# Optimization experiments

Measured on AMD Instinct MI355X. Metric: run time of the kernel, lower is better.

## Reference

```python
import jax, jax.numpy as jnp
import numpy as np

BN_EPS = 1e-5

def _bn(x, gamma, beta, relu=True):
    # training-mode BatchNorm over all dims except channel (last)
    axes = tuple(range(x.ndim - 1))
    mu = jnp.mean(x, axes, keepdims=True)
    var = jnp.var(x, axes, keepdims=True)
    y = (x - mu) / jnp.sqrt(var + BN_EPS) * gamma + beta
    return jax.nn.relu(y) if relu else y

def _l2norm(x, eps):
    # F.normalize: x / max(||x||, eps)
    n = jnp.sqrt(jnp.sum(x * x, axis=-1, keepdims=True))
    return x / jnp.maximum(n, eps)

def setup_inputs() -> dict:
    key = jax.random.key(0)
    ks = jax.random.split(key, 16)
    B, N, H, W, C = 2, 512, 16, 32, 64
    IN_DIM = 10 + C + C + 2  # 140
    MLP3 = [128, 64]
    s = 0.02
    inp = {
        "warped_xyz": jax.random.normal(ks[0], (B, N, 3), jnp.float32),
        "warped_points": jax.random.normal(ks[1], (B, N, C), jnp.float32),
        "RF3": jax.random.normal(ks[2], (B, C, H, W), jnp.float32),
        "RF3_index": jax.random.normal(ks[3], (B, 3, H, W), jnp.float32),
        "lidar_z": jax.random.uniform(ks[4], (B, N, 1), jnp.float32),
        # conv1x1 stack (mlp3)
        "W1": jax.random.normal(ks[5], (IN_DIM, MLP3[0]), jnp.float32) * s,
        "b1": jnp.zeros((MLP3[0],), jnp.float32),
        "g1": jnp.ones((MLP3[0],), jnp.float32),
        "be1": jnp.zeros((MLP3[0],), jnp.float32),
        "W2": jax.random.normal(ks[6], (MLP3[0], MLP3[1]), jnp.float32) * s,
        "b2": jnp.zeros((MLP3[1],), jnp.float32),
        "g2": jnp.ones((MLP3[1],), jnp.float32),
        "be2": jnp.zeros((MLP3[1],), jnp.float32),
        # conv1d stack (mlp4 = [feats_dim//2], then 2 logits)
        "M1w": jax.random.normal(ks[7], (MLP3[1], MLP3[1] // 2), jnp.float32) * s,
        "M1b": jnp.zeros((MLP3[1] // 2,), jnp.float32),
        "M1g": jnp.ones((MLP3[1] // 2,), jnp.float32),
        "M1be": jnp.zeros((MLP3[1] // 2,), jnp.float32),
        "M2w": jax.random.normal(ks[8], (MLP3[1] // 2, 2), jnp.float32) * s,
        "M2b": jnp.zeros((2,), jnp.float32),
    }
    return inp

def reference(warped_xyz, warped_points, RF3, RF3_index, lidar_z,
              W1, b1, g1, be1, W2, b2, g2, be2,
              M1w, M1b, M1g, M1be, M2w, M2b):
    B, N, _ = warped_xyz.shape
    _, Ci, H, W_ = RF3.shape
    M = H * W_
    RF3_bnc = RF3.transpose(0, 2, 3, 1).reshape(B, M, Ci)          # [B,M,C]
    idx_bnc = RF3_index.transpose(0, 2, 3, 1).reshape(B, M, 3)     # [B,M,3]

    src_xyz = warped_xyz[:, :, None, :]                             # [B,N,1,3]
    dst_xyz = idx_bnc[:, None, :, :]                                # [B,1,M,3]
    euc = (src_xyz - dst_xyz)[..., :2]                              # [B,N,M,2]
    euc_norm = jnp.sqrt(euc[..., 0:1] ** 2 + euc[..., 1:2] ** 2)    # [B,N,M,1]

    xyz_z = (warped_xyz * lidar_z)[:, :, None, :]                   # [B,N,1,3]
    src_pts = warped_points[:, :, None, :]                          # [B,N,1,C]
    dst_pts = RF3_bnc[:, None, :, :]                                # [B,1,M,C]

    geom = jnp.concatenate([
        jnp.broadcast_to(xyz_z, (B, N, M, 3)),
        jnp.broadcast_to(src_pts[..., :2], (B, N, M, 2)),
        jnp.broadcast_to(dst_xyz[..., :2], (B, N, M, 2)),
        euc, euc_norm], axis=-1)                                    # [B,N,M,10]
    desc = jnp.concatenate([
        jnp.broadcast_to(src_pts, (B, N, M, Ci)),
        jnp.broadcast_to(dst_pts, (B, N, M, Ci))], axis=-1)         # [B,N,M,2C]

    # cal_sim: cosine sim between lidar feats (src) and image feats (dst)
    src_n = _l2norm(warped_points, 1e-12)
    dst_n = _l2norm(RF3_bnc, 1e-12)
    cos = jnp.einsum('bnc,bmc->bnm', src_n, dst_n)                  # [B,N,M]
    s1 = cos / (jnp.max(cos, axis=2, keepdims=True) + 1e-6)         # src->dst norm
    s2 = cos / (jnp.max(cos, axis=1, keepdims=True) + 1e-10)        # dst->src norm
    sim = jnp.stack([s1, s2], axis=-1)                              # [B,N,M,2]

    feats = jnp.concatenate([geom, desc, sim], axis=-1)             # [B,N,M,140]
    feats = _bn(jnp.einsum('bnmi,io->bnmo', feats, W1) + b1, g1, be1)
    feats = _bn(jnp.einsum('bnmi,io->bnmo', feats, W2) + b2, g2, be2)

    aw = jax.nn.softmax(jnp.max(feats, axis=-1), axis=-1)           # [B,N,M]
    att = jnp.einsum('bnm,bnmc->bnc', aw, feats)                    # [B,N,C]

    att = _bn(att @ M1w + M1b, M1g, M1be)
    logits = att @ M2w + M2b                                        # [B,N,2]
    return logits
```

## Files before the change

kernel.cpp:

```cpp
#include <hip/hip_runtime.h>
#include <hip/hip_bf16.h>

#define B_ 2
#define N_ 512
#define M_ 512
#define C_ 64
#define O1 128
#define O2 64
#define O3 32
#define PBIG 524288.0f
#define P3   1024.0f

typedef short s8v __attribute__((ext_vector_type(8)));
typedef float f4v __attribute__((ext_vector_type(4)));

#define WS_SRCN 0
#define WS_DSTN 65536
#define WS_P0   0
#define WS_U    131072
#define WS_Z    131072
#define WS_V    262144
#define WS_DXY  393216
#define WS_COS  395264
#define WS_RMAX 919552
#define WS_ST1  920576
#define WS_ST2  936960
#define WS_ST3  945152
#define WS_CMAX 949248
#define WS_W2F  950272
#define WS_W9S  954368
#define WS_X2   961536

__device__ __forceinline__ unsigned short f2bf(float f){
  unsigned u = __float_as_uint(f);
  unsigned r = (u + 0x7fffu + ((u >> 16) & 1u)) >> 16;
  return (unsigned short)r;
}
__device__ __forceinline__ float bf2f(unsigned short h){
  return __uint_as_float(((unsigned)h) << 16);
}
__device__ __forceinline__ unsigned pk2(float lo, float hi){
  return (unsigned)f2bf(lo) | ((unsigned)f2bf(hi) << 16);
}
__device__ __forceinline__ unsigned pk_trunc(float lo, float hi){
  return __builtin_amdgcn_perm(__float_as_uint(hi), __float_as_uint(lo), 0x07060302u);
}
__device__ __forceinline__ f4v relu4(f4v z){
  z[0] = fmaxf(z[0], 0.f); z[1] = fmaxf(z[1], 0.f);
  z[2] = fmaxf(z[2], 0.f); z[3] = fmaxf(z[3], 0.f);
  return z;
}

__global__ __launch_bounds__(128) void k1(const float* __restrict__ wxyz,
    const float* __restrict__ wpts, const float* __restrict__ lz,
    const float* __restrict__ rf3, const float* __restrict__ rf3i,
    const float* __restrict__ W1, float* __restrict__ ws){
  int t = threadIdx.x;
  if (blockIdx.x < 1024){
    int blk = blockIdx.x; int b = blk >> 9, n = blk & 511;
    int bn = b*N_ + n;
    __shared__ float wp[64]; __shared__ float sxyz[3]; __shared__ float slz; __shared__ float srn;
    if (t < 64) wp[t] = wpts[bn*64 + t];
    if (t >= 64 && t < 67) sxyz[t-64] = wxyz[bn*3 + (t-64)];
    if (t == 67) slz = lz[bn];
    __syncthreads();
    if (t < 64){
      float v = wp[t]*wp[t];
      v += __shfl_down(v,32); v += __shfl_down(v,16); v += __shfl_down(v,8);
      v += __shfl_down(v,4);  v += __shfl_down(v,2);  v += __shfl_down(v,1);
      if (t == 0) srn = 1.0f / fmaxf(sqrtf(v), 1e-12f);
    }
    __syncthreads();
    if (t < 64) ws[WS_SRCN + bn*64 + t] = wp[t]*srn;
    int o = t;
    float x = sxyz[0], y = sxyz[1], z = sxyz[2], l = slz;
    float acc = x*l*W1[0*O1+o] + y*l*W1[1*O1+o] + z*l*W1[2*O1+o]
              + wp[0]*W1[3*O1+o] + wp[1]*W1[4*O1+o]
              + x*W1[7*O1+o] + y*W1[8*O1+o];
    #pragma unroll 8
    for (int c = 0; c < 64; ++c) acc += wp[c]*W1[(10+c)*O1+o];
    ws[WS_U + bn*O1 + o] = acc;
  } else {
    int blk = blockIdx.x - 1024; int b = blk >> 9, m = blk & 511;
    int bm = b*M_ + m;
    __shared__ float rf[64]; __shared__ float sdx, sdy, srn2;
    if (t < 64) rf[t] = rf3[(b*64 + t)*512 + m];
    if (t == 64) sdx = rf3i[(b*3 + 0)*512 + m];
    if (t == 65) sdy = rf3i[(b*3 + 1)*512 + m];
    __syncthreads();
    if (t < 64){
      float v = rf[t]*rf[t];
      v += __shfl_down(v,32); v += __shfl_down(v,16); v += __shfl_down(v,8);
      v += __shfl_down(v,4);  v += __shfl_down(v,2);  v += __shfl_down(v,1);
      if (t == 0) srn2 = 1.0f / fmaxf(sqrtf(v), 1e-12f);
    }
    __syncthreads();
    if (t < 64) ws[WS_DSTN + bm*64 + t] = rf[t]*srn2;
    if (t == 0){ ws[WS_DXY + bm*2+0] = sdx; ws[WS_DXY + bm*2+1] = sdy; }
    int o = t;
    float acc = sdx*(W1[5*O1+o] - W1[7*O1+o]) + sdy*(W1[6*O1+o] - W1[8*O1+o]);
    #pragma unroll 8
    for (int c = 0; c < 64; ++c) acc += rf[c]*W1[(74+c)*O1+o];
    ws[WS_V + bm*O1 + o] = acc;
  }
}

__global__ __launch_bounds__(256) void k2(float* __restrict__ ws){
  int blk = blockIdx.x; int b = blk >> 9, n = blk & 511; int t = threadIdx.x;
  int bn = b*N_ + n;
  __shared__ __align__(16) float sn[64];
  __shared__ float dnt[64*65];
  __shared__ float part[4*64];
  if (t < 64) sn[t] = ws[WS_SRCN + bn*64 + t];
  float lmax = -3.4e38f;
  for (int chunk = 0; chunk < 8; ++chunk){
    __syncthreads();
    const float4* src = (const float4*)(ws + WS_DSTN + (size_t)(b*M_ + chunk*64)*64);
    #pragma unroll
    for (int i = 0; i < 4; ++i){
      float4 v = src[t + i*256];
      int base = (t + i*256)*4; int mm = base >> 6, c = base & 63;
      float* dp = &dnt[mm*65 + c];
      dp[0]=v.x; dp[1]=v.y; dp[2]=v.z; dp[3]=v.w;
    }
    __syncthreads();
    {
      int mm = t & 63, cg = t >> 6;
      const float* dr = &dnt[mm*65 + cg*16];
      const float* sr = &sn[cg*16];
      float p = 0.f;
      #pragma unroll
      for (int k = 0; k < 16; ++k) p += sr[k]*dr[k];
      part[cg*64 + mm] = p;
    }
    __syncthreads();
    if (t < 64){
      float d = part[t] + part[64+t] + part[128+t] + part[192+t];
      ws[WS_COS + bn*M_ + chunk*64 + t] = d;
      lmax = fmaxf(lmax, d);
    }
  }
  if (t < 64){
    lmax = fmaxf(lmax, __shfl_xor(lmax,32)); lmax = fmaxf(lmax, __shfl_xor(lmax,16));
    lmax = fmaxf(lmax, __shfl_xor(lmax,8));  lmax = fmaxf(lmax, __shfl_xor(lmax,4));
    lmax = fmaxf(lmax, __shfl_xor(lmax,2));  lmax = fmaxf(lmax, __shfl_xor(lmax,1));
    if (t == 0) ws[WS_RMAX + bn] = 1.0f / (lmax + 1e-6f);
  }
}

__global__ __launch_bounds__(256) void k2r(float* __restrict__ ws){
  int blk = blockIdx.x;
  int b = blk >> 4; int c0 = (blk & 15)*32;
  int t = threadIdx.x;
  int col = c0 + (t & 31), seg = t >> 5;
  float mx = -3.4e38f;
  #pragma unroll 8
  for (int i = 0; i < 64; ++i){
    int n = seg*64 + i;
    mx = fmaxf(mx, ws[WS_COS + (size_t)(b*N_ + n)*M_ + col]);
  }
  __shared__ float sred[256];
  sred[t] = mx;
  __syncthreads();
  if (t < 32){
    float m2 = sred[t];
    #pragma unroll
    for (int s2 = 1; s2 < 8; ++s2) m2 = fmaxf(m2, sred[s2*32 + t]);
    ws[WS_CMAX + b*M_ + c0 + t] = 1.0f / (m2 + 1e-10f);
  }
}

__global__ __launch_bounds__(256) void k3(const float* __restrict__ wxyz,
    const float* __restrict__ W1, const float* __restrict__ b1, float* __restrict__ ws){
  int blk = blockIdx.x; int bn = blk >> 1, half = blk & 1; int t = threadIdx.x;
  int b = bn >> 9; int mbase = half*256;
  __shared__ float s_en[256], s_s1[256], s_s2[256];
  __shared__ float sred[512];
  float sx = wxyz[bn*3+0], sy = wxyz[bn*3+1];
  float ri = ws[WS_RMAX + bn];
  {
    int m = mbase + t;
    float2 d = *(const float2*)(ws + WS_DXY + (size_t)(b*M_+m)*2);
    float ex = sx-d.x, ey = sy-d.y;
    s_en[t] = sqrtf(ex*ex + ey*ey);
    float cv = ws[WS_COS + (size_t)bn*M_ + m];
    s_s1[t] = cv*ri;
    s_s2[t] = cv*ws[WS_CMAX + b*M_ + m];
  }
  __syncthreads();
  int o = t & 127, mh = t >> 7;
  float u  = ws[WS_U + bn*O1 + o] + b1[o];
  float w9 = W1[9*O1+o], wa = W1[138*O1+o], wb = W1[139*O1+o];
  float sum = 0.f, ssq = 0.f;
  const float* Vp = ws + WS_V + (size_t)b*M_*O1 + o;
  int lBeg = mh*128, lEnd = lBeg + 128;
  #pragma unroll 8
  for (int ml = lBeg; ml < lEnd; ++ml){
    float xv = u + Vp[(size_t)(mbase+ml)*O1] + s_en[ml]*w9 + s_s1[ml]*wa + s_s2[ml]*wb;
    sum += xv; ssq += xv*xv;
  }
  sred[mh*128 + o] = sum;
  sred[256 + mh*128 + o] = ssq;
  __syncthreads();
  if (t < 128){
    float S = sred[t] + sred[128+t];
    float Q = sred[256+t] + sred[384+t];
    int rep = blk & 63;
    atomicAdd(&ws[WS_ST1 + rep*256 + t], S);
    atomicAdd(&ws[WS_ST1 + rep*256 + 128 + t], Q);
  }
}

__global__ __launch_bounds__(128) void k3b(const float* __restrict__ W1,
    const float* __restrict__ b1, const float* __restrict__ g1,
    const float* __restrict__ be1, const float* __restrict__ W2, float* __restrict__ ws){
  int blk = blockIdx.x; int t = threadIdx.x;
  int o = t;
  float s = 0.f, q = 0.f;
  #pragma unroll 8
  for (int r = 0; r < 64; ++r){ s += ws[WS_ST1 + r*256 + o]; q += ws[WS_ST1 + r*256 + 128 + o]; }
  float mu = s/PBIG, var = q/PBIG - mu*mu;
  float istd = rsqrtf(var + 1e-5f);
  float A1 = g1[o]*istd, C1 = be1[o] - mu*A1;
  if (blk < 1024){
    int bn = blk;
    ws[WS_P0 + bn*O1 + o] = (ws[WS_U + bn*O1 + o] + b1[o])*A1 + C1;
  } else if (blk < 1040){
    int r0 = (blk - 1024)*64;
    for (int r = 0; r < 64; ++r)
      ws[WS_V + (size_t)(r0 + r)*O1 + o] *= A1;
  } else {
    ws[WS_W9S + o]       = W1[9*O1+o]*A1;
    ws[WS_W9S + 128 + o] = W1[138*O1+o]*A1;
    ws[WS_W9S + 256 + o] = W1[139*O1+o]*A1;
    unsigned short* wf = (unsigned short*)(ws + WS_W2F);
    for (int i = t; i < 8192; i += 128){
      int j = i & 7, ll = (i >> 3) & 63, ct = (i >> 9) & 3, k0q = i >> 11;
      int oo = k0q*32 + (ll >> 4)*8 + j, c = ct*16 + (ll & 15);
      wf[i] = f2bf(W2[oo*O2 + c]);
    }
  }
}

__global__ __launch_bounds__(256, 4) void k4(const float* __restrict__ wxyz,
    float* __restrict__ ws){
  int blk = blockIdx.x; int bn = blk >> 1, half = blk & 1;
  int b = bn >> 9; int t = threadIdx.x;
  __shared__ __align__(16) unsigned short wBf[8192];
  __shared__ __align__(16) float p0s[128], w9s[128], was[128], wbs[128];
  __shared__ float ls[64], lq[64];
  {
    const s8v* g = (const s8v*)(ws + WS_W2F);
    s8v* l = (s8v*)wBf;
    #pragma unroll
    for (int c2 = 0; c2 < 4; ++c2) l[c2*256 + t] = g[c2*256 + t];
  }
  if (t < 64){ ls[t] = 0.f; lq[t] = 0.f; }
  if (t < 128){
    p0s[t] = ws[WS_P0 + bn*O1 + t];
    w9s[t] = ws[WS_W9S + t];
    was[t] = ws[WS_W9S + 128 + t];
    wbs[t] = ws[WS_W9S + 256 + t];
  }
  __syncthreads();
  int ll = t & 63, w = t >> 6, l16 = ll & 15, quad = ll >> 4;
  float sx = wxyz[bn*3+0], sy = wxyz[bn*3+1];
  float ri = ws[WS_RMAX + bn];
  float sst[4][4], sq2[4][4];
  #pragma unroll
  for (int i = 0; i < 4; ++i)
    #pragma unroll
    for (int j = 0; j < 4; ++j){ sst[i][j] = 0.f; sq2[i][j] = 0.f; }
  uint4* xf4 = (uint4*)(ws + WS_X2) + (size_t)bn*4096;
  union U8 { s8v v; unsigned u[4]; };
  #pragma unroll
  for (int mci = 0; mci < 2; ++mci){
    int mc = half*2 + mci;
    int mA = mc*128 + w*32 + l16, mB = mA + 16;
    float2 dA = *(const float2*)(ws + WS_DXY + (size_t)(b*M_+mA)*2);
    float2 dB = *(const float2*)(ws + WS_DXY + (size_t)(b*M_+mB)*2);
    float cvA = ws[WS_COS + (size_t)bn*M_ + mA], cvB = ws[WS_COS + (size_t)bn*M_ + mB];
    float ciA = ws[WS_CMAX + b*M_ + mA],         ciB = ws[WS_CMAX + b*M_ + mB];
    float exA = sx-dA.x, eyA = sy-dA.y; float en0 = sqrtf(exA*exA + eyA*eyA);
    float exB = sx-dB.x, eyB = sy-dB.y; float en1 = sqrtf(exB*exB + eyB*eyB);
    float s10 = cvA*ri, s20 = cvA*ciA;
    float s11 = cvB*ri, s21 = cvB*ciB;
    const float* vpA = ws + WS_V + (size_t)(b*M_+mA)*O1;
    const float* vpB = ws + WS_V + (size_t)(b*M_+mB)*O1;
    f4v acc[2][4];
    #pragma unroll
    for (int i = 0; i < 2; ++i)
      #pragma unroll
      for (int j = 0; j < 4; ++j) acc[i][j] = (f4v){0.f,0.f,0.f,0.f};
    #pragma unroll
    for (int k0q = 0; k0q < 4; ++k0q){
      int ko = k0q*32 + quad*8;
      f4v p0a = *(const f4v*)&p0s[ko], p0b = *(const f4v*)&p0s[ko+4];
      f4v w9a = *(const f4v*)&w9s[ko], w9b = *(const f4v*)&w9s[ko+4];
      f4v waa = *(const f4v*)&was[ko], wab = *(const f4v*)&was[ko+4];
      f4v wba = *(const f4v*)&wbs[ko], wbb = *(const f4v*)&wbs[ko+4];
      f4v vA0 = *(const f4v*)(vpA + ko), vA1 = *(const f4v*)(vpA + ko + 4);
      f4v vB0 = *(const f4v*)(vpB + ko), vB1 = *(const f4v*)(vpB + ko + 4);
      f4v zaA = relu4(p0a + vA0 + en0*w9a + s10*waa + s20*wba);
      f4v zbA = relu4(p0b + vA1 + en0*w9b + s10*wab + s20*wbb);
      f4v zaB = relu4(p0a + vB0 + en1*w9a + s11*waa + s21*wba);
      f4v zbB = relu4(p0b + vB1 + en1*w9b + s11*wab + s21*wbb);
      U8 uA, uB;
      uA.u[0] = pk_trunc(zaA[0], zaA[1]); uA.u[1] = pk_trunc(zaA[2], zaA[3]);
      uA.u[2] = pk_trunc(zbA[0], zbA[1]); uA.u[3] = pk_trunc(zbA[2], zbA[3]);
      uB.u[0] = pk_trunc(zaB[0], zaB[1]); uB.u[1] = pk_trunc(zaB[2], zaB[3]);
      uB.u[2] = pk_trunc(zbB[0], zbB[1]); uB.u[3] = pk_trunc(zbB[2], zbB[3]);
      #pragma unroll
      for (int ct = 0; ct < 4; ++ct){
        s8v bb = *(const s8v*)&wBf[((k0q*4 + ct)*64 + ll)*8];
        acc[0][ct] = __builtin_amdgcn_mfma_f32_16x16x32_bf16(bb, uA.v, acc[0][ct], 0,0,0);
        acc[1][ct] = __builtin_amdgcn_mfma_f32_16x16x32_bf16(bb, uB.v, acc[1][ct], 0,0,0);
      }
    }
    #pragma unroll
    for (int mt = 0; mt < 2; ++mt){
      uint4 u0, u1;
      u0.x = pk2(acc[mt][0][0], acc[mt][0][1]); u0.y = pk2(acc[mt][0][2], acc[mt][0][3]);
      u0.z = pk2(acc[mt][1][0], acc[mt][1][1]); u0.w = pk2(acc[mt][1][2], acc[mt][1][3]);
      u1.x = pk2(acc[mt][2][0], acc[mt][2][1]); u1.y = pk2(acc[mt][2][2], acc[mt][2][3]);
      u1.z = pk2(acc[mt][3][0], acc[mt][3][1]); u1.w = pk2(acc[mt][3][2], acc[mt][3][3]);
      xf4[((((mc*4 + w)*2 + mt)*2 + 0)*64) + ll] = u0;
      xf4[((((mc*4 + w)*2 + mt)*2 + 1)*64) + ll] = u1;
    }
    #pragma unroll
    for (int ct = 0; ct < 4; ++ct)
      #pragma unroll
      for (int r = 0; r < 4; ++r){
        float a0 = acc[0][ct][r], a1 = acc[1][ct][r];
        sst[ct][r] += a0 + a1;
        sq2[ct][r] += a0*a0 + a1*a1;
      }
  }
  #pragma unroll
  for (int ct = 0; ct < 4; ++ct){
    #pragma unroll
    for (int r = 0; r < 4; ++r){
      float s = sst[ct][r], q = sq2[ct][r];
      s += __shfl_xor(s,1); s += __shfl_xor(s,2); s += __shfl_xor(s,4); s += __shfl_xor(s,8);
      q += __shfl_xor(q,1); q += __shfl_xor(q,2); q += __shfl_xor(q,4); q += __shfl_xor(q,8);
      if (l16 == 0){
        atomicAdd(&ls[ct*16 + quad*4 + r], s);
        atomicAdd(&lq[ct*16 + quad*4 + r], q);
      }
    }
  }
  __syncthreads();
  int rep = blk & 63;
  if (t < 64) atomicAdd(&ws[WS_ST2 + rep*128 + t], ls[t]);
  else if (t < 128) atomicAdd(&ws[WS_ST2 + rep*128 + t], lq[t-64]);
}

__global__ __launch_bounds__(256) void k5(const float* __restrict__ g2,
    const float* __restrict__ be2, const float* __restrict__ M1w,
    const float* __restrict__ M1b, float* __restrict__ ws){
  int bn = blockIdx.x; int t = threadIdx.x;
  __shared__ float sa2[64], sc2[64];
  __shared__ float s_mx[512];
  __shared__ float s_aw[512];
  __shared__ float red[256];
  __shared__ float part[64*65];
  __shared__ float s_att[64];
  __shared__ float sgmax, sinvS;
  if (t < 64){
    float s = 0.f, q = 0.f;
    #pragma unroll 8
    for (int r = 0; r < 64; ++r){ s += ws[WS_ST2 + r*128 + t]; q += ws[WS_ST2 + r*128 + 64 + t]; }
    float mu = s/PBIG, var = q/PBIG - mu*mu;
    float istd = rsqrtf(var + 1e-5f);
    float A2 = g2[t]*istd;
    sa2[t] = A2; sc2[t] = be2[t] - mu*A2;
  }
  __syncthreads();
  int ll = t & 63, w = t >> 6, l16 = ll & 15, quad = ll >> 4;
  const uint4* xf4 = (const uint4*)(ws + WS_X2) + (size_t)bn*4096;
  uint4 xv[4][2][2];
  #pragma unroll
  for (int mc = 0; mc < 4; ++mc)
    #pragma unroll
    for (int mt = 0; mt < 2; ++mt)
      #pragma unroll
      for (int cp = 0; cp < 2; ++cp)
        xv[mc][mt][cp] = xf4[((((mc*4 + w)*2 + mt)*2 + cp)*64) + ll];
  float a2r[4][4], c2r[4][4];
  #pragma unroll
  for (int ct = 0; ct < 4; ++ct)
    #pragma unroll
    for (int r = 0; r < 4; ++r){
      int c = ct*16 + quad*4 + r;
      a2r[ct][r] = sa2[c]; c2r[ct][r] = sc2[c];
    }
  #pragma unroll
  for (int mc = 0; mc < 4; ++mc){
    #pragma unroll
    for (int mt = 0; mt < 2; ++mt){
      float mx = 0.f;
      #pragma unroll
      for (int cp = 0; cp < 2; ++cp){
        uint4 uv = xv[mc][mt][cp];
        int c0t = 2*cp, c1t = 2*cp + 1;
        float x0 = bf2f((unsigned short)(uv.x & 0xffffu));
        float x1 = bf2f((unsigned short)(uv.x >> 16));
        float x2 = bf2f((unsigned short)(uv.y & 0xffffu));
        float x3 = bf2f((unsigned short)(uv.y >> 16));
        float x4 = bf2f((unsigned short)(uv.z & 0xffffu));
        float x5 = bf2f((unsigned short)(uv.z >> 16));
        float x6 = bf2f((unsigned short)(uv.w & 0xffffu));
        float x7 = bf2f((unsigned short)(uv.w >> 16));
        mx = fmaxf(mx, a2r[c0t][0]*x0 + c2r[c0t][0]);
        mx = fmaxf(mx, a2r[c0t][1]*x1 + c2r[c0t][1]);
        mx = fmaxf(mx, a2r[c0t][2]*x2 + c2r[c0t][2]);
        mx = fmaxf(mx, a2r[c0t][3]*x3 + c2r[c0t][3]);
        mx = fmaxf(mx, a2r[c1t][0]*x4 + c2r[c1t][0]);
        mx = fmaxf(mx, a2r[c1t][1]*x5 + c2r[c1t][1]);
        mx = fmaxf(mx, a2r[c1t][2]*x6 + c2r[c1t][2]);
        mx = fmaxf(mx, a2r[c1t][3]*x7 + c2r[c1t][3]);
      }
      mx = fmaxf(mx, __shfl_xor(mx,16));
      mx = fmaxf(mx, __shfl_xor(mx,32));
      if (quad == 0) s_mx[mc*128 + w*32 + mt*16 + l16] = mx;
    }
  }
  __syncthreads();
  red[t] = fmaxf(s_mx[t], s_mx[t+256]);
  __syncthreads();
  for (int s = 128; s > 0; s >>= 1){ if (t < s) red[t] = fmaxf(red[t], red[t+s]); __syncthreads(); }
  if (t == 0) sgmax = red[0];
  __syncthreads();
  float e0 = expf(s_mx[t] - sgmax), e1 = expf(s_mx[t+256] - sgmax);
  s_aw[t] = e0; s_aw[t+256] = e1;
  red[t] = e0 + e1;
  __syncthreads();
  for (int s = 128; s > 0; s >>= 1){ if (t < s) red[t] += red[t+s]; __syncthreads(); }
  if (t == 0) sinvS = 1.0f / red[0];
  __syncthreads();
  float acc[4][4];
  #pragma unroll
  for (int ct = 0; ct < 4; ++ct)
    #pragma unroll
    for (int r = 0; r < 4; ++r) acc[ct][r] = 0.f;
  #pragma unroll
  for (int mc = 0; mc < 4; ++mc){
    #pragma unroll
    for (int mt = 0; mt < 2; ++mt){
      float aw = s_aw[mc*128 + w*32 + mt*16 + l16];
      #pragma unroll
      for (int cp = 0; cp < 2; ++cp){
        uint4 uv = xv[mc][mt][cp];
        int c0t = 2*cp, c1t = 2*cp + 1;
        float x0 = bf2f((unsigned short)(uv.x & 0xffffu));
        float x1 = bf2f((unsigned short)(uv.x >> 16));
        float x2 = bf2f((unsigned short)(uv.y & 0xffffu));
        float x3 = bf2f((unsigned short)(uv.y >> 16));
        float x4 = bf2f((unsigned short)(uv.z & 0xffffu));
        float x5 = bf2f((unsigned short)(uv.z >> 16));
        float x6 = bf2f((unsigned short)(uv.w & 0xffffu));
        float x7 = bf2f((unsigned short)(uv.w >> 16));
        acc[c0t][0] += aw*fmaxf(a2r[c0t][0]*x0 + c2r[c0t][0], 0.f);
        acc[c0t][1] += aw*fmaxf(a2r[c0t][1]*x1 + c2r[c0t][1], 0.f);
        acc[c0t][2] += aw*fmaxf(a2r[c0t][2]*x2 + c2r[c0t][2], 0.f);
        acc[c0t][3] += aw*fmaxf(a2r[c0t][3]*x3 + c2r[c0t][3], 0.f);
        acc[c1t][0] += aw*fmaxf(a2r[c1t][0]*x4 + c2r[c1t][0], 0.f);
        acc[c1t][1] += aw*fmaxf(a2r[c1t][1]*x5 + c2r[c1t][1], 0.f);
        acc[c1t][2] += aw*fmaxf(a2r[c1t][2]*x6 + c2r[c1t][2], 0.f);
        acc[c1t][3] += aw*fmaxf(a2r[c1t][3]*x7 + c2r[c1t][3], 0.f);
      }
    }
  }
  int row = w*16 + l16;
  #pragma unroll
  for (int ct = 0; ct < 4; ++ct)
    #pragma unroll
    for (int r = 0; r < 4; ++r)
      part[row*65 + ct*16 + quad*4 + r] = acc[ct][r];
  __syncthreads();
  if (t < 64){
    float a = 0.f;
    #pragma unroll 8
    for (int r = 0; r < 64; ++r) a += part[r*65 + t];
    s_att[t] = a * sinvS;
  }
  __syncthreads();
  if (t < 32){
    float z = M1b[t];
    #pragma unroll 8
    for (int c = 0; c < 64; ++c) z += s_att[c]*M1w[c*32 + t];
    ws[WS_Z + bn*32 + t] = z;
    int rep = bn & 63;
    atomicAdd(&ws[WS_ST3 + rep*64 + t], z);
    atomicAdd(&ws[WS_ST3 + rep*64 + 32 + t], z*z);
  }
}

__global__ __launch_bounds__(256) void k6(const float* __restrict__ M1g,
    const float* __restrict__ M1be, const float* __restrict__ M2w,
    const float* __restrict__ M2b, const float* __restrict__ ws, float* __restrict__ out){
  int t = threadIdx.x; int s = blockIdx.x*256 + t;
  __shared__ float sa3[32], sc3[32];
  if (t < 32){
    float su = 0.f, q = 0.f;
    #pragma unroll 8
    for (int r = 0; r < 64; ++r){ su += ws[WS_ST3 + r*64 + t]; q += ws[WS_ST3 + r*64 + 32 + t]; }
    float mu = su/P3, var = q/P3 - mu*mu;
    float istd = rsqrtf(var + 1e-5f);
    float A3 = M1g[t]*istd;
    sa3[t] = A3; sc3[t] = M1be[t] - mu*A3;
  }
  __syncthreads();
  float a0 = M2b[0], a1 = M2b[1];
  #pragma unroll
  for (int j = 0; j < 32; ++j){
    float y = fmaxf(ws[WS_Z + s*32 + j]*sa3[j] + sc3[j], 0.f);
    a0 += y*M2w[j*2+0]; a1 += y*M2w[j*2+1];
  }
  out[s*2+0] = a0; out[s*2+1] = a1;
}

extern "C" void kernel_launch(void* const* d_in, const int* in_sizes, int n_in,
                              void* d_out, int out_size, void* d_ws, size_t ws_size,
                              hipStream_t stream){
  const float* wxyz = (const float*)d_in[0];
  const float* wpts = (const float*)d_in[1];
  const float* rf3  = (const float*)d_in[2];
  const float* rf3i = (const float*)d_in[3];
  const float* lz   = (const float*)d_in[4];
  const float* W1   = (const float*)d_in[5];
  const float* b1   = (const float*)d_in[6];
  const float* g1   = (const float*)d_in[7];
  const float* be1  = (const float*)d_in[8];
  const float* W2   = (const float*)d_in[9];
  const float* g2   = (const float*)d_in[11];
  const float* be2  = (const float*)d_in[12];
  const float* M1w  = (const float*)d_in[13];
  const float* M1b  = (const float*)d_in[14];
  const float* M1g  = (const float*)d_in[15];
  const float* M1be = (const float*)d_in[16];
  const float* M2w  = (const float*)d_in[17];
  const float* M2b  = (const float*)d_in[18];
  float* ws  = (float*)d_ws;
  float* out = (float*)d_out;
  hipMemsetAsync(ws + WS_ST1, 0, 28672*sizeof(float), stream);
  k1 <<<2048,128,0,stream>>>(wxyz, wpts, lz, rf3, rf3i, W1, ws);
  k2 <<<1024,256,0,stream>>>(ws);
  k2r<<<32,256,0,stream>>>(ws);
  k3 <<<2048,256,0,stream>>>(wxyz, W1, b1, ws);
  k3b<<<1041,128,0,stream>>>(W1, b1, g1, be1, W2, ws);
  k4 <<<2048,256,0,stream>>>(wxyz, ws);
  k5 <<<1024,256,0,stream>>>(g2, be2, M1w, M1b, ws);
  k6 <<<4,256,0,stream>>>(M1g, M1be, M2w, M2b, ws, out);
}
```

Measured before the change: 232.6 us.

## Compute layer-1 BN statistics algebraically from row/column moments instead of full pass

Replaces the full N×M×128 pass for the first BatchNorm's mean and variance with an algebraic decomposition. It uses per-row and per-column moments of u, v, distance and similarity terms, plus cross terms, combined in a new per-channel kernel. k2r now also computes column sums, k3a computes per-row moments, and k3s assembles the statistics. k4 is also split into four blocks per point instead of two to raise parallelism. The risk is precision loss from the expanded variance formula and cancellation in the cross terms.

New measurement: 218.0 us. 1.07x faster.

```diff
diff --git a/kernel.cpp b/kernel.cpp
--- a/kernel.cpp
+++ b/kernel.cpp
@@ -23,7 +23,10 @@
 #define WS_DXY  393216
 #define WS_COS  395264
 #define WS_RMAX 919552
-#define WS_ST1  920576
+#define WS_ROWS 920576
+#define WS_COLS 923648
+#define WS_A1C  926720
+#define WS_SC2P 935936
 #define WS_ST2  936960
 #define WS_ST3  945152
 #define WS_CMAX 949248
@@ -148,86 +151,158 @@
   }
 }
 
-__global__ __launch_bounds__(256) void k2r(float* __restrict__ ws){
+__global__ __launch_bounds__(256) void k2r(const float* __restrict__ wxyz, float* __restrict__ ws){
   int blk = blockIdx.x;
-  int b = blk >> 4; int c0 = (blk & 15)*32;
+  int b = blk >> 5; int c0 = (blk & 31)*16;
   int t = threadIdx.x;
-  int col = c0 + (t & 31), seg = t >> 5;
-  float mx = -3.4e38f;
-  #pragma unroll 8
-  for (int i = 0; i < 64; ++i){
-    int n = seg*64 + i;
-    mx = fmaxf(mx, ws[WS_COS + (size_t)(b*N_ + n)*M_ + col]);
-  }
-  __shared__ float sred[256];
-  sred[t] = mx;
-  __syncthreads();
-  if (t < 32){
-    float m2 = sred[t];
-    #pragma unroll
-    for (int s2 = 1; s2 < 8; ++s2) m2 = fmaxf(m2, sred[s2*32 + t]);
-    ws[WS_CMAX + b*M_ + c0 + t] = 1.0f / (m2 + 1e-10f);
-  }
-}
-
-__global__ __launch_bounds__(256) void k3(const float* __restrict__ wxyz,
-    const float* __restrict__ W1, const float* __restrict__ b1, float* __restrict__ ws){
-  int blk = blockIdx.x; int bn = blk >> 1, half = blk & 1; int t = threadIdx.x;
-  int b = bn >> 9; int mbase = half*256;
-  __shared__ float s_en[256], s_s1[256], s_s2[256];
-  __shared__ float sred[512];
+  int cl = t & 15, seg = t >> 4;
+  int col = c0 + cl;
+  int bm = b*M_ + col;
+  float dx = ws[WS_DXY + bm*2+0], dy = ws[WS_DXY + bm*2+1];
+  float mx = -3.4e38f, se = 0.f, sc = 0.f, s1c = 0.f;
+  for (int i = 0; i < 32; ++i){
+    int bn = b*N_ + seg*32 + i;
+    float cv = ws[WS_COS + (size_t)bn*M_ + col];
+    float ri = ws[WS_RMAX + bn];
+    float sx = wxyz[bn*3+0], sy = wxyz[bn*3+1];
+    float ex = sx-dx, ey = sy-dy;
+    se += sqrtf(ex*ex + ey*ey);
+    mx = fmaxf(mx, cv);
+    sc += cv;
+    s1c += cv*ri;
+  }
+  __shared__ float r0[256], r1[256], r2[256], r3[256];
+  r0[t]=mx; r1[t]=se; r2[t]=s1c; r3[t]=sc;
+  __syncthreads();
+  for (int s = 8; s > 0; s >>= 1){
+    if (seg < s){
+      int o2 = t + s*16;
+      r0[t] = fmaxf(r0[t], r0[o2]); r1[t] += r1[o2]; r2[t] += r2[o2]; r3[t] += r3[o2];
+    }
+    __syncthreads();
+  }
+  if (t < 16){
+    int bmw = b*M_ + c0 + t;
+    float ci = 1.0f/(r0[t] + 1e-10f);
+    ws[WS_CMAX + bmw] = ci;
+    ws[WS_COLS + bmw] = r1[t];
+    ws[WS_COLS + 1024 + bmw] = r2[t];
+    ws[WS_COLS + 2048 + bmw] = r3[t]*ci;
+  }
+}
+
+__global__ __launch_bounds__(256) void k3a(const float* __restrict__ wxyz, float* __restrict__ ws){
+  int bn = blockIdx.x; int b = bn >> 9; int t = threadIdx.x;
+  float ri = ws[WS_RMAX + bn];
   float sx = wxyz[bn*3+0], sy = wxyz[bn*3+1];
-  float ri = ws[WS_RMAX + bn];
-  {
-    int m = mbase + t;
+  float q[9];
+  #pragma unroll
+  for (int j = 0; j < 9; ++j) q[j] = 0.f;
+  #pragma unroll
+  for (int k = 0; k < 2; ++k){
+    int m = t + k*256;
     float2 d = *(const float2*)(ws + WS_DXY + (size_t)(b*M_+m)*2);
     float ex = sx-d.x, ey = sy-d.y;
-    s_en[t] = sqrtf(ex*ex + ey*ey);
+    float en = sqrtf(ex*ex + ey*ey);
     float cv = ws[WS_COS + (size_t)bn*M_ + m];
-    s_s1[t] = cv*ri;
-    s_s2[t] = cv*ws[WS_CMAX + b*M_ + m];
-  }
-  __syncthreads();
-  int o = t & 127, mh = t >> 7;
-  float u  = ws[WS_U + bn*O1 + o] + b1[o];
-  float w9 = W1[9*O1+o], wa = W1[138*O1+o], wb = W1[139*O1+o];
-  float sum = 0.f, ssq = 0.f;
-  const float* Vp = ws + WS_V + (size_t)b*M_*O1 + o;
-  int lBeg = mh*128, lEnd = lBeg + 128;
-  #pragma unroll 8
-  for (int ml = lBeg; ml < lEnd; ++ml){
-    float xv = u + Vp[(size_t)(mbase+ml)*O1] + s_en[ml]*w9 + s_s1[ml]*wa + s_s2[ml]*wb;
-    sum += xv; ssq += xv*xv;
-  }
-  sred[mh*128 + o] = sum;
-  sred[256 + mh*128 + o] = ssq;
-  __syncthreads();
-  if (t < 128){
-    float S = sred[t] + sred[128+t];
-    float Q = sred[256+t] + sred[384+t];
-    int rep = blk & 63;
-    atomicAdd(&ws[WS_ST1 + rep*256 + t], S);
-    atomicAdd(&ws[WS_ST1 + rep*256 + 128 + t], Q);
+    float ci = ws[WS_CMAX + b*M_ + m];
+    float s2 = cv*ci;
+    q[0]+=en; q[1]+=cv; q[2]+=s2; q[3]+=en*en; q[4]+=cv*cv; q[5]+=s2*s2;
+    q[6]+=en*cv; q[7]+=en*s2; q[8]+=cv*cv*ci;
+  }
+  #pragma unroll
+  for (int j = 0; j < 9; ++j){
+    float v = q[j];
+    v += __shfl_xor(v,1); v += __shfl_xor(v,2); v += __shfl_xor(v,4);
+    v += __shfl_xor(v,8); v += __shfl_xor(v,16); v += __shfl_xor(v,32);
+    q[j] = v;
+  }
+  __shared__ float wr[9][4];
+  int w = t >> 6;
+  if ((t & 63) == 0){
+    #pragma unroll
+    for (int j = 0; j < 9; ++j) wr[j][w] = q[j];
+  }
+  __syncthreads();
+  if (t < 9){
+    float Q = wr[t][0] + wr[t][1] + wr[t][2] + wr[t][3];
+    float f = (t==1 || t==6 || t==8) ? ri : ((t==4) ? ri*ri : 1.0f);
+    float s = f*Q;
+    if (t < 3) ws[WS_ROWS + t*1024 + bn] = s;
+    atomicAdd(&ws[WS_SC2P + (bn & 63)*16 + t], s);
+  }
+}
+
+__global__ __launch_bounds__(256) void k3s(const float* __restrict__ W1,
+    const float* __restrict__ b1, const float* __restrict__ g1,
+    const float* __restrict__ be1, float* __restrict__ ws){
+  int o = blockIdx.x; int t = threadIdx.x;
+  __shared__ float scal[9];
+  __shared__ float wr[12][4];
+  if (t < 9){
+    float s = 0.f;
+    #pragma unroll 8
+    for (int r = 0; r < 64; ++r) s += ws[WS_SC2P + r*16 + t];
+    scal[t] = s;
+  }
+  float b1o = b1[o];
+  float a[12];
+  #pragma unroll
+  for (int j = 0; j < 12; ++j) a[j] = 0.f;
+  #pragma unroll
+  for (int k = 0; k < 4; ++k){
+    int i = t + k*256;
+    float u = ws[WS_U + (size_t)i*O1 + o] + b1o;
+    float v = ws[WS_V + (size_t)i*O1 + o];
+    float ren = ws[WS_ROWS + i], rs1 = ws[WS_ROWS + 1024 + i], rs2 = ws[WS_ROWS + 2048 + i];
+    float cen = ws[WS_COLS + i], cs1 = ws[WS_COLS + 1024 + i], cs2 = ws[WS_COLS + 2048 + i];
+    a[0]+=u; a[1]+=u*u; a[2]+=u*ren; a[3]+=u*rs1; a[4]+=u*rs2;
+    a[5]+=v; a[6]+=v*v; a[7]+=v*cen; a[8]+=v*cs1; a[9]+=v*cs2;
+    if (k < 2){ a[10]+=u; a[11]+=v; }
+  }
+  #pragma unroll
+  for (int j = 0; j < 12; ++j){
+    float v = a[j];
+    v += __shfl_xor(v,1); v += __shfl_xor(v,2); v += __shfl_xor(v,4);
+    v += __shfl_xor(v,8); v += __shfl_xor(v,16); v += __shfl_xor(v,32);
+    a[j] = v;
+  }
+  int w = t >> 6;
+  if ((t & 63) == 0){
+    #pragma unroll
+    for (int j = 0; j < 12; ++j) wr[j][w] = a[j];
+  }
+  __syncthreads();
+  if (t == 0){
+    float A[12];
+    #pragma unroll
+    for (int j = 0; j < 12; ++j) A[j] = wr[j][0] + wr[j][1] + wr[j][2] + wr[j][3];
+    float w9 = W1[9*O1+o], wa = W1[138*O1+o], wb = W1[139*O1+o];
+    float S1 = 512.f*(A[0] + A[5]) + w9*scal[0] + wa*scal[1] + wb*scal[2];
+    float Q1 = 512.f*(A[1] + A[6])
+      + 2.f*(A[10]*A[11] + (A[0]-A[10])*(A[5]-A[11]))
+      + w9*w9*scal[3] + wa*wa*scal[4] + wb*wb*scal[5]
+      + 2.f*(w9*wa*scal[6] + w9*wb*scal[7] + wa*wb*scal[8])
+      + 2.f*(w9*A[2] + wa*A[3] + wb*A[4])
+      + 2.f*(w9*A[7] + wa*A[8] + wb*A[9]);
+    float mu = S1/PBIG, var = Q1/PBIG - mu*mu;
+    float istd = rsqrtf(var + 1e-5f);
+    float A1v = g1[o]*istd;
+    ws[WS_A1C + o] = A1v;
+    ws[WS_A1C + 128 + o] = be1[o] - mu*A1v;
   }
 }
 
 __global__ __launch_bounds__(128) void k3b(const float* __restrict__ W1,
-    const float* __restrict__ b1, const float* __restrict__ g1,
-    const float* __restrict__ be1, const float* __restrict__ W2, float* __restrict__ ws){
-  int blk = blockIdx.x; int t = threadIdx.x;
-  int o = t;
-  float s = 0.f, q = 0.f;
-  #pragma unroll 8
-  for (int r = 0; r < 64; ++r){ s += ws[WS_ST1 + r*256 + o]; q += ws[WS_ST1 + r*256 + 128 + o]; }
-  float mu = s/PBIG, var = q/PBIG - mu*mu;
-  float istd = rsqrtf(var + 1e-5f);
-  float A1 = g1[o]*istd, C1 = be1[o] - mu*A1;
+    const float* __restrict__ b1, const float* __restrict__ W2, float* __restrict__ ws){
+  int blk = blockIdx.x; int t = threadIdx.x; int o = t;
+  float A1 = ws[WS_A1C + o], C1 = ws[WS_A1C + 128 + o];
   if (blk < 1024){
-    int bn = blk;
-    ws[WS_P0 + bn*O1 + o] = (ws[WS_U + bn*O1 + o] + b1[o])*A1 + C1;
-  } else if (blk < 1040){
-    int r0 = (blk - 1024)*64;
-    for (int r = 0; r < 64; ++r)
+    ws[WS_P0 + blk*O1 + o] = (ws[WS_U + blk*O1 + o] + b1[o])*A1 + C1;
+  } else if (blk < 1088){
+    int r0 = (blk - 1024)*16;
+    #pragma unroll
+    for (int r = 0; r < 16; ++r)
       ws[WS_V + (size_t)(r0 + r)*O1 + o] *= A1;
   } else {
     ws[WS_W9S + o]       = W1[9*O1+o]*A1;
@@ -244,7 +319,7 @@
 
 __global__ __launch_bounds__(256, 4) void k4(const float* __restrict__ wxyz,
     float* __restrict__ ws){
-  int blk = blockIdx.x; int bn = blk >> 1, half = blk & 1;
+  int blk = blockIdx.x; int bn = blk >> 2, mc = blk & 3;
   int b = bn >> 9; int t = threadIdx.x;
   __shared__ __align__(16) unsigned short wBf[8192];
   __shared__ __align__(16) float p0s[128], w9s[128], was[128], wbs[128];
@@ -266,81 +341,66 @@
   int ll = t & 63, w = t >> 6, l16 = ll & 15, quad = ll >> 4;
   float sx = wxyz[bn*3+0], sy = wxyz[bn*3+1];
   float ri = ws[WS_RMAX + bn];
-  float sst[4][4], sq2[4][4];
-  #pragma unroll
-  for (int i = 0; i < 4; ++i)
-    #pragma unroll
-    for (int j = 0; j < 4; ++j){ sst[i][j] = 0.f; sq2[i][j] = 0.f; }
   uint4* xf4 = (uint4*)(ws + WS_X2) + (size_t)bn*4096;
   union U8 { s8v v; unsigned u[4]; };
-  #pragma unroll
-  for (int mci = 0; mci < 2; ++mci){
-    int mc = half*2 + mci;
-    int mA = mc*128 + w*32 + l16, mB = mA + 16;
-    float2 dA = *(const float2*)(ws + WS_DXY + (size_t)(b*M_+mA)*2);
-    float2 dB = *(const float2*)(ws + WS_DXY + (size_t)(b*M_+mB)*2);
-    float cvA = ws[WS_COS + (size_t)bn*M_ + mA], cvB = ws[WS_COS + (size_t)bn*M_ + mB];
-    float ciA = ws[WS_CMAX + b*M_ + mA],         ciB = ws[WS_CMAX + b*M_ + mB];
-    float exA = sx-dA.x, eyA = sy-dA.y; float en0 = sqrtf(exA*exA + eyA*eyA);
-    float exB = sx-dB.x, eyB = sy-dB.y; float en1 = sqrtf(exB*exB + eyB*eyB);
-    float s10 = cvA*ri, s20 = cvA*ciA;
-    float s11 = cvB*ri, s21 = cvB*ciB;
-    const float* vpA = ws + WS_V + (size_t)(b*M_+mA)*O1;
-    const float* vpB = ws + WS_V + (size_t)(b*M_+mB)*O1;
-    f4v acc[2][4];
-    #pragma unroll
-    for (int i = 0; i < 2; ++i)
-      #pragma unroll
-      for (int j = 0; j < 4; ++j) acc[i][j] = (f4v){0.f,0.f,0.f,0.f};
-    #pragma unroll
-    for (int k0q = 0; k0q < 4; ++k0q){
-      int ko = k0q*32 + quad*8;
-      f4v p0a = *(const f4v*)&p0s[ko], p0b = *(const f4v*)&p0s[ko+4];
-      f4v w9a = *(const f4v*)&w9s[ko], w9b = *(const f4v*)&w9s[ko+4];
-      f4v waa = *(const f4v*)&was[ko], wab = *(const f4v*)&was[ko+4];
-      f4v wba = *(const f4v*)&wbs[ko], wbb = *(const f4v*)&wbs[ko+4];
-      f4v vA0 = *(const f4v*)(vpA + ko), vA1 = *(const f4v*)(vpA + ko + 4);
-      f4v vB0 = *(const f4v*)(vpB + ko), vB1 = *(const f4v*)(vpB + ko + 4);
-      f4v zaA = relu4(p0a + vA0 + en0*w9a + s10*waa + s20*wba);
-      f4v zbA = relu4(p0b + vA1 + en0*w9b + s10*wab + s20*wbb);
-      f4v zaB = relu4(p0a + vB0 + en1*w9a + s11*waa + s21*wba);
-      f4v zbB = relu4(p0b + vB1 + en1*w9b + s11*wab + s21*wbb);
-      U8 uA, uB;
-      uA.u[0] = pk_trunc(zaA[0], zaA[1]); uA.u[1] = pk_trunc(zaA[2], zaA[3]);
-      uA.u[2] = pk_trunc(zbA[0], zbA[1]); uA.u[3] = pk_trunc(zbA[2], zbA[3]);
-      uB.u[0] = pk_trunc(zaB[0], zaB[1]); uB.u[1] = pk_trunc(zaB[2], zaB[3]);
-      uB.u[2] = pk_trunc(zbB[0], zbB[1]); uB.u[3] = pk_trunc(zbB[2], zbB[3]);
-      #pragma unroll
-      for (int ct = 0; ct < 4; ++ct){
-        s8v bb = *(const s8v*)&wBf[((k0q*4 + ct)*64 + ll)*8];
-        acc[0][ct] = __builtin_amdgcn_mfma_f32_16x16x32_bf16(bb, uA.v, acc[0][ct], 0,0,0);
-        acc[1][ct] = __builtin_amdgcn_mfma_f32_16x16x32_bf16(bb, uB.v, acc[1][ct], 0,0,0);
-      }
-    }
-    #pragma unroll
-    for (int mt = 0; mt < 2; ++mt){
-      uint4 u0, u1;
-      u0.x = pk2(acc[mt][0][0], acc[mt][0][1]); u0.y = pk2(acc[mt][0][2], acc[mt][0][3]);
-      u0.z = pk2(acc[mt][1][0], acc[mt][1][1]); u0.w = pk2(acc[mt][1][2], acc[mt][1][3]);
-      u1.x = pk2(acc[mt][2][0], acc[mt][2][1]); u1.y = pk2(acc[mt][2][2], acc[mt][2][3]);
-      u1.z = pk2(acc[mt][3][0], acc[mt][3][1]); u1.w = pk2(acc[mt][3][2], acc[mt][3][3]);
-      xf4[((((mc*4 + w)*2 + mt)*2 + 0)*64) + ll] = u0;
-      xf4[((((mc*4 + w)*2 + mt)*2 + 1)*64) + ll] = u1;
-    }
-    #pragma unroll
-    for (int ct = 0; ct < 4; ++ct)
-      #pragma unroll
-      for (int r = 0; r < 4; ++r){
-        float a0 = acc[0][ct][r], a1 = acc[1][ct][r];
-        sst[ct][r] += a0 + a1;
-        sq2[ct][r] += a0*a0 + a1*a1;
-      }
+  int mA = mc*128 + w*32 + l16, mB = mA + 16;
+  float2 dA = *(const float2*)(ws + WS_DXY + (size_t)(b*M_+mA)*2);
+  float2 dB = *(const float2*)(ws + WS_DXY + (size_t)(b*M_+mB)*2);
+  float cvA = ws[WS_COS + (size_t)bn*M_ + mA], cvB = ws[WS_COS + (size_t)bn*M_ + mB];
+  float ciA = ws[WS_CMAX + b*M_ + mA],         ciB = ws[WS_CMAX + b*M_ + mB];
+  float exA = sx-dA.x, eyA = sy-dA.y; float en0 = sqrtf(exA*exA + eyA*eyA);
+  float exB = sx-dB.x, eyB = sy-dB.y; float en1 = sqrtf(exB*exB + eyB*eyB);
+  float s10 = cvA*ri, s20 = cvA*ciA;
+  float s11 = cvB*ri, s21 = cvB*ciB;
+  const float* vpA = ws + WS_V + (size_t)(b*M_+mA)*O1;
+  const float* vpB = ws + WS_V + (size_t)(b*M_+mB)*O1;
+  f4v acc[2][4];
+  #pragma unroll
+  for (int i = 0; i < 2; ++i)
+    #pragma unroll
+    for (int j = 0; j < 4; ++j) acc[i][j] = (f4v){0.f,0.f,0.f,0.f};
+  #pragma unroll
+  for (int k0q = 0; k0q < 4; ++k0q){
+    int ko = k0q*32 + quad*8;
+    f4v p0a = *(const f4v*)&p0s[ko], p0b = *(const f4v*)&p0s[ko+4];
+    f4v w9a = *(const f4v*)&w9s[ko], w9b = *(const f4v*)&w9s[ko+4];
+    f4v waa = *(const f4v*)&was[ko], wab = *(const f4v*)&was[ko+4];
+    f4v wba = *(const f4v*)&wbs[ko], wbb = *(const f4v*)&wbs[ko+4];
+    f4v vA0 = *(const f4v*)(vpA + ko), vA1 = *(const f4v*)(vpA + ko + 4);
+    f4v vB0 = *(const f4v*)(vpB + ko), vB1 = *(const f4v*)(vpB + ko + 4);
+    f4v zaA = relu4(p0a + vA0 + en0*w9a + s10*waa + s20*wba);
+    f4v zbA = relu4(p0b + vA1 + en0*w9b + s10*wab + s20*wbb);
+    f4v zaB = relu4(p0a + vB0 + en1*w9a + s11*waa + s21*wba);
+    f4v zbB = relu4(p0b + vB1 + en1*w9b + s11*wab + s21*wbb);
+    U8 uA, uB;
+    uA.u[0] = pk_trunc(zaA[0], zaA[1]); uA.u[1] = pk_trunc(zaA[2], zaA[3]);
+    uA.u[2] = pk_trunc(zbA[0], zbA[1]); uA.u[3] = pk_trunc(zbA[2], zbA[3]);
+    uB.u[0] = pk_trunc(zaB[0], zaB[1]); uB.u[1] = pk_trunc(zaB[2], zaB[3]);
+    uB.u[2] = pk_trunc(zbB[0], zbB[1]); uB.u[3] = pk_trunc(zbB[2], zbB[3]);
+    #pragma unroll
+    for (int ct = 0; ct < 4; ++ct){
+      s8v bb = *(const s8v*)&wBf[((k0q*4 + ct)*64 + ll)*8];
+      acc[0][ct] = __builtin_amdgcn_mfma_f32_16x16x32_bf16(bb, uA.v, acc[0][ct], 0,0,0);
+      acc[1][ct] = __builtin_amdgcn_mfma_f32_16x16x32_bf16(bb, uB.v, acc[1][ct], 0,0,0);
+    }
+  }
+  #pragma unroll
+  for (int mt = 0; mt < 2; ++mt){
+    uint4 u0, u1;
+    u0.x = pk2(acc[mt][0][0], acc[mt][0][1]); u0.y = pk2(acc[mt][0][2], acc[mt][0][3]);
+    u0.z = pk2(acc[mt][1][0], acc[mt][1][1]); u0.w = pk2(acc[mt][1][2], acc[mt][1][3]);
+    u1.x = pk2(acc[mt][2][0], acc[mt][2][1]); u1.y = pk2(acc[mt][2][2], acc[mt][2][3]);
+    u1.z = pk2(acc[mt][3][0], acc[mt][3][1]); u1.w = pk2(acc[mt][3][2], acc[mt][3][3]);
+    xf4[((((mc*4 + w)*2 + mt)*2 + 0)*64) + ll] = u0;
+    xf4[((((mc*4 + w)*2 + mt)*2 + 1)*64) + ll] = u1;
   }
   #pragma unroll
   for (int ct = 0; ct < 4; ++ct){
     #pragma unroll
     for (int r = 0; r < 4; ++r){
-      float s = sst[ct][r], q = sq2[ct][r];
+      float a0 = acc[0][ct][r], a1 = acc[1][ct][r];
+      float s = a0 + a1;
+      float q = a0*a0 + a1*a1;
       s += __shfl_xor(s,1); s += __shfl_xor(s,2); s += __shfl_xor(s,4); s += __shfl_xor(s,8);
       q += __shfl_xor(q,1); q += __shfl_xor(q,2); q += __shfl_xor(q,4); q += __shfl_xor(q,8);
       if (l16 == 0){
@@ -543,13 +603,14 @@
   const float* M2b  = (const float*)d_in[18];
   float* ws  = (float*)d_ws;
   float* out = (float*)d_out;
-  hipMemsetAsync(ws + WS_ST1, 0, 28672*sizeof(float), stream);
+  hipMemsetAsync(ws + WS_SC2P, 0, 13312*sizeof(float), stream);
   k1 <<<2048,128,0,stream>>>(wxyz, wpts, lz, rf3, rf3i, W1, ws);
   k2 <<<1024,256,0,stream>>>(ws);
-  k2r<<<32,256,0,stream>>>(ws);
-  k3 <<<2048,256,0,stream>>>(wxyz, W1, b1, ws);
-  k3b<<<1041,128,0,stream>>>(W1, b1, g1, be1, W2, ws);
-  k4 <<<2048,256,0,stream>>>(wxyz, ws);
+  k2r<<<64,256,0,stream>>>(wxyz, ws);
+  k3a<<<1024,256,0,stream>>>(wxyz, ws);
+  k3s<<<128,256,0,stream>>>(W1, b1, g1, be1, ws);
+  k3b<<<1089,128,0,stream>>>(W1, b1, W2, ws);
+  k4 <<<4096,256,0,stream>>>(wxyz, ws);
   k5 <<<1024,256,0,stream>>>(g2, be2, M1w, M1b, ws);
   k6 <<<4,256,0,stream>>>(M1g, M1be, M2w, M2b, ws, out);
 }
```
